# Performance work log

Hardware: AMD Instinct MI355X
Metric: run time of the kernel (lower is better)

## Reference

```python
import jax, jax.numpy as jnp
import numpy as np

N, K, D, H, F = 4, 2048, 512, 8, 2048
Dh = D // H  # per-head dim_q = dim_v = dim_out = 64
EPS = 1e-10


def _uinit(k, shape, fan_sum):
    c = (6.0 / fan_sum) ** 0.5
    return jax.random.uniform(k, shape, jnp.float32, -c, c)


def setup_inputs() -> dict:
    key = jax.random.key(0)
    ks = jax.random.split(key, 8)
    x = jax.random.normal(ks[0], (N, K, D), jnp.float32)
    # per-head projection weights, stacked over heads: (H, D, Dh)
    Wq = _uinit(ks[1], (H, D, Dh), D + Dh)
    Wk = _uinit(ks[2], (H, D, Dh), D + Dh)
    Wv = _uinit(ks[3], (H, D, Dh), D + Dh)
    bq = jnp.zeros((H, Dh), jnp.float32)
    bk = jnp.zeros((H, Dh), jnp.float32)
    bv = jnp.zeros((H, Dh), jnp.float32)
    Wo = _uinit(ks[4], (H * Dh, D), H * Dh + D)
    bo = jnp.zeros((D,), jnp.float32)
    W1 = _uinit(ks[5], (D, F), D + F)
    b1 = jnp.zeros((F,), jnp.float32)
    W2 = _uinit(ks[6], (F, D), F + D)
    b2 = jnp.zeros((D,), jnp.float32)
    g1 = jnp.ones((D,), jnp.float32)
    be1 = jnp.zeros((D,), jnp.float32)
    g2 = jnp.ones((D,), jnp.float32)
    be2 = jnp.zeros((D,), jnp.float32)
    # causal mask: True = masked position (masked_fill semantics)
    mask = jnp.broadcast_to(jnp.triu(jnp.ones((K, K), bool), 1), (N, K, K))
    return dict(x=x, Wq=Wq, bq=bq, Wk=Wk, bk=bk, Wv=Wv, bv=bv, Wo=Wo, bo=bo,
                W1=W1, b1=b1, W2=W2, b2=b2, g1=g1, be1=be1, g2=g2, be2=be2,
                mask=mask)


def _layer_norm(x, g, b):
    m = x.mean(-1, keepdims=True)
    v = ((x - m) ** 2).mean(-1, keepdims=True)
    return g * (x - m) / jnp.sqrt(v + EPS) + b


def _block(x, Wq, bq, Wk, bk, Wv, bv, Wo, bo, W1, b1, W2, b2, g1, be1, g2, be2, mask):
    # per-head projections: (N, H, K, Dh)
    q = jnp.einsum('nkd,hde->nhke', x, Wq) + bq[None, :, None, :]
    k = jnp.einsum('nkd,hde->nhke', x, Wk) + bk[None, :, None, :]
    v = jnp.einsum('nkd,hde->nhke', x, Wv) + bv[None, :, None, :]
    # full score matrix (N, H, K, K) -- faithful to bmm-softmax-bmm
    s = jnp.einsum('nhqe,nhke->nhqk', q, k) / (Dh ** 0.5)
    s = jnp.where(mask[:, None], -1e9, s)
    w = jax.nn.softmax(s, axis=-1)
    att = jnp.einsum('nhqk,nhke->nhqe', w, v)
    att = att.transpose(0, 2, 1, 3).reshape(N, K, H * Dh)  # concat heads
    att = att @ Wo + bo
    h1 = _layer_norm(x + att, g1, be1)
    ff = jax.nn.relu(h1 @ W1 + b1) @ W2 + b2
    return _layer_norm(h1 + ff, g2, be2)


def reference(x, Wq, bq, Wk, bk, Wv, bv, Wo, bo, W1, b1, W2, b2, g1, be1, g2, be2, mask):
    return _block(x, Wq, bq, Wk, bk, Wv, bv, Wo, bo, W1, b1, W2, b2, g1, be1, g2, be2, mask)
```

## Files before the change

### kernel.cpp

```cpp
#include <hip/hip_runtime.h>
#include <cstdint>

typedef unsigned short u16;
typedef __bf16 bf16x8 __attribute__((ext_vector_type(8)));
typedef float f32x4 __attribute__((ext_vector_type(4)));
struct __align__(8) U2 { unsigned x, y; };

#define NEG_INF (-__builtin_inff())

__device__ __forceinline__ u16 f2bf(float f) {
  unsigned u = __builtin_bit_cast(unsigned, f);
  u += 0x7FFFu + ((u >> 16) & 1u);
  return (u16)(u >> 16);
}
__device__ __forceinline__ float bf2f(u16 b) {
  unsigned u = (unsigned)b << 16;
  return __builtin_bit_cast(float, u);
}
__device__ __forceinline__ u16 bfbits(__bf16 x) { return __builtin_bit_cast(u16, x); }
__device__ __forceinline__ unsigned pk2(float a, float b) {
  u16 lo = bfbits((__bf16)a), hi = bfbits((__bf16)b);
  return (unsigned)lo | ((unsigned)hi << 16);
}

__device__ __forceinline__ void async16(u16* dst, const u16* src) {
  __builtin_amdgcn_global_load_lds(
      (__attribute__((address_space(1))) void*)(u16*)src,
      (__attribute__((address_space(3))) void*)dst, 16, 0, 0);
}

__global__ __launch_bounds__(256) void k_prep(const float* __restrict__ Wo,
                                              const float* __restrict__ W1,
                                              const float* __restrict__ W2,
                                              const float* __restrict__ Wq,
                                              const float* __restrict__ Wk,
                                              const float* __restrict__ Wv,
                                              const float* __restrict__ bq,
                                              const float* __restrict__ bk,
                                              const float* __restrict__ bv,
                                              const float* __restrict__ x,
                                              u16* __restrict__ WoT,
                                              u16* __restrict__ W1T,
                                              u16* __restrict__ W2T,
                                              u16* __restrict__ WqkvT,
                                              float* __restrict__ bqkv,
                                              u16* __restrict__ xb) {
  const int b = blockIdx.x, tid = threadIdx.x;
  if (b >= 1542) {
    int i = (b - 1542) * 256 + tid;
    const float4* in = (const float4*)x;
    float4 a = in[2 * i], c = in[2 * i + 1];
    uint4 r;
    r.x = (unsigned)f2bf(a.x) | ((unsigned)f2bf(a.y) << 16);
    r.y = (unsigned)f2bf(a.z) | ((unsigned)f2bf(a.w) << 16);
    r.z = (unsigned)f2bf(c.x) | ((unsigned)f2bf(c.y) << 16);
    r.w = (unsigned)f2bf(c.z) | ((unsigned)f2bf(c.w) << 16);
    ((uint4*)xb)[i] = r;
    return;
  }
  if (b >= 1536) {
    int i = (b - 1536) * 256 + tid;
    int m = i >> 9, r = i & 511;
    const float* B = (m == 0) ? bq : (m == 1) ? bk : bv;
    bqkv[i] = B[r];
    return;
  }
  __shared__ float t[32][65];
  const float* ip;
  u16* op;
  int R, C, r0, c0;
  if (b < 128)      { ip = Wo; op = WoT; R = 512;  C = 512;  c0 = (b & 7) * 64;          r0 = (b >> 3) * 32; }
  else if (b < 640) { int i = b - 128; ip = W1; op = W1T; R = 512;  C = 2048; c0 = (i & 31) * 64; r0 = (i >> 5) * 32; }
  else if (b < 1152){ int i = b - 640; ip = W2; op = W2T; R = 2048; C = 512;  c0 = (i & 7) * 64;  r0 = (i >> 3) * 32; }
  else {
    int i = b - 1152;
    int z = i >> 4;
    const float* W = (z < 8) ? Wq : (z < 16) ? Wk : Wv;
    ip = W + (size_t)(z & 7) * 32768;
    op = WqkvT + (size_t)z * 32768;
    R = 512; C = 64; c0 = 0; r0 = (i & 15) * 32;
  }
  int tx = tid & 63, ty = tid >> 6;
#pragma unroll
  for (int i = 0; i < 32; i += 4)
    t[ty + i][tx] = ip[(size_t)(r0 + ty + i) * C + c0 + tx];
  __syncthreads();
  int cx = tid & 31, cy = tid >> 5;
#pragma unroll
  for (int j = 0; j < 64; j += 8)
    op[(size_t)(c0 + cy + j) * R + r0 + cx] = f2bf(t[cx][cy + j]);
}

template <bool DBUF, int EPI, int BN>
__global__ __launch_bounds__(256) void k_gemm(const u16* __restrict__ A,
                                              const u16* __restrict__ BT,
                                              const float* __restrict__ bias,
                                              u16* __restrict__ Cout,
                                              int M, int N, int Kd) {
  constexpr int HALF = 8192 + BN * 64;
  __shared__ __align__(16) u16 lds[DBUF ? 2 * HALF : HALF];
  constexpr int NFR = BN / 32;
  constexpr int BITER = BN / 32;
  const int tid = threadIdx.x, wid = tid >> 6, lane = tid & 63;
  const int lr = lane & 15, lg = lane >> 4;
  const int wr = wid >> 1, wc = wid & 1;
  const int bid = blockIdx.x;
  const int xcd = bid & 7, local = bid >> 3;
  const int tm = (xcd * 8 + (local & 7)) * 128;
  const int tn = (local >> 3) * BN;

  f32x4 acc[4][NFR] = {};

  const int srow = lane >> 3;
  const int kb = (lane & 7) ^ srow;

  auto STAGE = [&](int buf, int kt) {
    u16* base = lds + buf * HALF;
#pragma unroll
    for (int it = 0; it < 4; ++it) {
      int rid = wid * 4 + it;
      int row = rid * 8 + srow;
      async16(base + rid * 512, A + (size_t)(tm + row) * Kd + kt + kb * 8);
    }
#pragma unroll
    for (int it = 0; it < BITER; ++it) {
      int rid = wid * BITER + it;
      int row = rid * 8 + srow;
      async16(base + 8192 + rid * 512, BT + (size_t)(tn + row) * Kd + kt + kb * 8);
    }
  };

  auto COMPUTE = [&](const char* lp) {
#pragma unroll
    for (int ks = 0; ks < 2; ++ks) {
      const int kbyte = ks * 64 + lg * 16;
      bf16x8 af[4], bfr[NFR];
#pragma unroll
      for (int mi = 0; mi < 4; ++mi) {
        int row = wr * 64 + mi * 16 + lr;
        af[mi] = *(const bf16x8*)(lp + row * 128 + (kbyte ^ ((row & 7) << 4)));
      }
#pragma unroll
      for (int nj = 0; nj < NFR; ++nj) {
        int row = wc * (BN / 2) + nj * 16 + lr;
        bfr[nj] = *(const bf16x8*)(lp + 16384 + row * 128 + (kbyte ^ ((row & 7) << 4)));
      }
#pragma unroll
      for (int mi = 0; mi < 4; ++mi)
#pragma unroll
        for (int nj = 0; nj < NFR; ++nj)
          acc[mi][nj] = __builtin_amdgcn_mfma_f32_16x16x32_bf16(af[mi], bfr[nj], acc[mi][nj], 0, 0, 0);
    }
  };

  const int nkt = Kd >> 6;
  if constexpr (DBUF) {
    STAGE(0, 0);
    for (int ki = 0; ki < nkt; ++ki) {
      __builtin_amdgcn_s_barrier();
      if (ki + 1 < nkt) {
        STAGE((ki + 1) & 1, (ki + 1) << 6);
        if constexpr (BN == 128) asm volatile("s_waitcnt vmcnt(8)" ::: "memory");
        else                     asm volatile("s_waitcnt vmcnt(6)" ::: "memory");
      } else {
        asm volatile("s_waitcnt vmcnt(0)" ::: "memory");
      }
      __builtin_amdgcn_s_barrier();
      __builtin_amdgcn_sched_barrier(0);
      COMPUTE((const char*)(lds + (ki & 1) * HALF));
    }
  } else {
    for (int ki = 0; ki < nkt; ++ki) {
      STAGE(0, ki << 6);
      __syncthreads();
      COMPUTE((const char*)lds);
      __syncthreads();
    }
  }

#pragma unroll
  for (int mi = 0; mi < 4; ++mi)
#pragma unroll
    for (int nj = 0; nj < NFR; ++nj) {
      int col = tn + wc * (BN / 2) + nj * 16 + lr;
      float bv = bias[col];
#pragma unroll
      for (int r = 0; r < 4; ++r) {
        int row = tm + wr * 64 + mi * 16 + lg * 4 + r;
        float v = acc[mi][nj][r] + bv;
        if (EPI == 1) v = v > 0.f ? v : 0.f;
        Cout[(size_t)row * N + col] = f2bf(v);
      }
    }
}

__global__ __launch_bounds__(256) void k_attn(const u16* __restrict__ QKV,
                                              u16* __restrict__ att) {
  __shared__ __align__(16) u16 lds[36864];
  const int lin = blockIdx.x;
  const int L = (lin & 7) * 64 + (lin >> 3);
  const int p = L & 15, nh = L >> 4;
  const int n = nh >> 3, h = nh & 7;
  const int tid = threadIdx.x, wid = tid >> 6, lane = tid & 63;
  const int lr = lane & 15, lg = lane >> 4;
  char* lp = (char*)lds;
  const u16* Qp = QKV + (size_t)(n * 2048) * 1536 + h * 64;
  const u16* Kp = Qp + 512;
  const u16* Vp = Qp + 1024;

  const int vkv = (tid & 31) * 2;
  const int vd0 = (tid >> 5) * 8;
  const int pwb = 65536 + wid * 2048;
  const float C2 = 0.18033688011112042f;
  const float B0 = 14.426950408889634f;

  for (int ph = 0; ph < 2; ++ph) {
    const int qc = (ph == 0) ? p : 31 - p;
    const int ntiles = qc + 1;
    const int qw = qc * 64 + wid * 16;
    const int qa = qw + lr;

    bf16x8 qf[2];
#pragma unroll
    for (int ks = 0; ks < 2; ++ks)
      qf[ks] = *(const bf16x8*)(Qp + (size_t)(qw + lr) * 1536 + ks * 32 + lg * 8);

    f32x4 o[4] = {};
    float lpart = 0.f;

    auto STAGE_K = [&](int t, int b) {
      const int kv0 = t * 64;
#pragma unroll
      for (int it = 0; it < 2; ++it) {
        int c = (wid * 2 + it) * 64 + lane;
        int row = c >> 3, ce = ((c & 7) ^ (row & 7)) * 8;
        async16(&lds[b * 4096 + (wid * 2 + it) * 512],
                Kp + (size_t)(kv0 + row) * 1536 + ce);
      }
    };
    auto VLAND = [&](bf16x8 va, bf16x8 vb, int b) {
#pragma unroll
      for (int jj = 0; jj < 8; ++jj) {
        int d = vd0 + jj;
        unsigned pk = (unsigned)bfbits(va[jj]) | ((unsigned)bfbits(vb[jj]) << 16);
        *(unsigned*)(lp + 32768 + b * 8192 + d * 128 + ((vkv * 2) ^ ((d & 7) << 4))) = pk;
      }
    };
    auto COMPUTE = [&](int t, int b) {
      const int kv0 = t * 64;
      f32x4 s[4] = {};
      __builtin_amdgcn_s_setprio(1);
#pragma unroll
      for (int nj = 0; nj < 4; ++nj) {
        int row = nj * 16 + lr;
#pragma unroll
        for (int ks = 0; ks < 2; ++ks) {
          bf16x8 kf = *(const bf16x8*)(lp + b * 8192 + row * 128 +
                                       ((ks * 64 + lg * 16) ^ ((row & 7) << 4)));
          s[nj] = __builtin_amdgcn_mfma_f32_16x16x32_bf16(kf, qf[ks], s[nj], 0, 0, 0);
        }
      }
      __builtin_amdgcn_s_setprio(0);

      if (t == ntiles - 1) {
#pragma unroll
        for (int nj = 0; nj < 4; ++nj) {
          int kvb = kv0 + nj * 16 + lg * 4;
#pragma unroll
          for (int r = 0; r < 4; ++r)
            if (kvb + r > qa) s[nj][r] = NEG_INF;
        }
      }

      float psum = 0.f;
#pragma unroll
      for (int nj = 0; nj < 4; ++nj)
#pragma unroll
        for (int r = 0; r < 4; ++r) {
          float pv = exp2f(fmaf(s[nj][r], C2, -B0));
          s[nj][r] = pv;
          psum += pv;
        }
      lpart += psum;

#pragma unroll
      for (int nj = 0; nj < 4; ++nj) {
        U2 val;
        val.x = pk2(s[nj][0], s[nj][1]);
        val.y = pk2(s[nj][2], s[nj][3]);
        *(U2*)(lp + pwb + lr * 128 + ((nj * 32 + lg * 8) ^ ((lr & 7) << 4))) = val;
      }

      bf16x8 pa[2];
#pragma unroll
      for (int ks = 0; ks < 2; ++ks)
        pa[ks] = *(const bf16x8*)(lp + pwb + lr * 128 +
                                  ((ks * 64 + lg * 16) ^ ((lr & 7) << 4)));
      __builtin_amdgcn_s_setprio(1);
#pragma unroll
      for (int nd = 0; nd < 4; ++nd) {
        int row = nd * 16 + lr;
#pragma unroll
        for (int ks = 0; ks < 2; ++ks) {
          bf16x8 vf = *(const bf16x8*)(lp + 32768 + b * 8192 + row * 128 +
                                       ((ks * 64 + lg * 16) ^ ((row & 7) << 4)));
          o[nd] = __builtin_amdgcn_mfma_f32_16x16x32_bf16(vf, pa[ks], o[nd], 0, 0, 0);
        }
      }
      __builtin_amdgcn_s_setprio(0);
    };

    STAGE_K(0, 0);
    if (ntiles > 1) STAGE_K(1, 1);
    {
      bf16x8 v0 = *(const bf16x8*)(Vp + (size_t)vkv * 1536 + vd0);
      bf16x8 v1 = *(const bf16x8*)(Vp + (size_t)(vkv + 1) * 1536 + vd0);
      VLAND(v0, v1, 0);
      if (ntiles > 1) {
        bf16x8 v2 = *(const bf16x8*)(Vp + (size_t)(64 + vkv) * 1536 + vd0);
        bf16x8 v3 = *(const bf16x8*)(Vp + (size_t)(64 + vkv + 1) * 1536 + vd0);
        VLAND(v2, v3, 1);
      }
    }
    __syncthreads();

    for (int t = 0; t < ntiles; t += 2) {
      const bool pre0 = (t + 2 < ntiles);
      const bool pre1 = (t + 3 < ntiles);
      bf16x8 va0, vb0, va1, vb1;
      if (pre0) {
        STAGE_K(t + 2, (t + 2) & 3);
        va0 = *(const bf16x8*)(Vp + (size_t)((t + 2) * 64 + vkv) * 1536 + vd0);
        vb0 = *(const bf16x8*)(Vp + (size_t)((t + 2) * 64 + vkv + 1) * 1536 + vd0);
      }
      if (pre1) {
        STAGE_K(t + 3, (t + 3) & 3);
        va1 = *(const bf16x8*)(Vp + (size_t)((t + 3) * 64 + vkv) * 1536 + vd0);
        vb1 = *(const bf16x8*)(Vp + (size_t)((t + 3) * 64 + vkv + 1) * 1536 + vd0);
      }

      COMPUTE(t, t & 3);
      if (t + 1 < ntiles) COMPUTE(t + 1, (t + 1) & 3);

      if (pre0) VLAND(va0, vb0, (t + 2) & 3);
      if (pre1) VLAND(va1, vb1, (t + 3) & 3);
      __syncthreads();
    }

    float lsum = lpart;
    lsum += __shfl_xor(lsum, 16);
    lsum += __shfl_xor(lsum, 32);
    float li = 1.0f / lsum;

    u16* ap = att + (size_t)(n * 2048 + qw + lr) * 512 + h * 64 + lg * 4;
#pragma unroll
    for (int nd = 0; nd < 4; ++nd) {
      U2 val;
      val.x = pk2(o[nd][0] * li, o[nd][1] * li);
      val.y = pk2(o[nd][2] * li, o[nd][3] * li);
      *(U2*)(ap + nd * 16) = val;
    }
  }
}

template <bool XF32>
__global__ __launch_bounds__(256) void k_add_ln(const void* __restrict__ Xp,
                                                const u16* __restrict__ Yb,
                                                const float* __restrict__ gam,
                                                const float* __restrict__ bet,
                                                float* __restrict__ outf,
                                                u16* __restrict__ outb) {
  const int wid = threadIdx.x >> 6, lane = threadIdx.x & 63;
  const size_t row = (size_t)blockIdx.x * 4 + wid;
  float xv[8];
  if constexpr (XF32) {
    const float4* x = (const float4*)((const float*)Xp + row * 512);
    float4 a0 = x[lane], a1 = x[lane + 64];
    xv[0] = a0.x; xv[1] = a0.y; xv[2] = a0.z; xv[3] = a0.w;
    xv[4] = a1.x; xv[5] = a1.y; xv[6] = a1.z; xv[7] = a1.w;
  } else {
    const u16* x = (const u16*)Xp + row * 512;
    U2 x0 = *(const U2*)(x + lane * 4);
    U2 x1 = *(const U2*)(x + 256 + lane * 4);
    xv[0] = bf2f((u16)(x0.x & 0xFFFF)); xv[1] = bf2f((u16)(x0.x >> 16));
    xv[2] = bf2f((u16)(x0.y & 0xFFFF)); xv[3] = bf2f((u16)(x0.y >> 16));
    xv[4] = bf2f((u16)(x1.x & 0xFFFF)); xv[5] = bf2f((u16)(x1.x >> 16));
    xv[6] = bf2f((u16)(x1.y & 0xFFFF)); xv[7] = bf2f((u16)(x1.y >> 16));
  }
  U2 y0 = *(const U2*)(Yb + row * 512 + lane * 4);
  U2 y1 = *(const U2*)(Yb + row * 512 + 256 + lane * 4);
  float v[8];
  v[0] = xv[0] + bf2f((u16)(y0.x & 0xFFFF));
  v[1] = xv[1] + bf2f((u16)(y0.x >> 16));
  v[2] = xv[2] + bf2f((u16)(y0.y & 0xFFFF));
  v[3] = xv[3] + bf2f((u16)(y0.y >> 16));
  v[4] = xv[4] + bf2f((u16)(y1.x & 0xFFFF));
  v[5] = xv[5] + bf2f((u16)(y1.x >> 16));
  v[6] = xv[6] + bf2f((u16)(y1.y & 0xFFFF));
  v[7] = xv[7] + bf2f((u16)(y1.y >> 16));
  float s = 0.f, ss = 0.f;
#pragma unroll
  for (int i = 0; i < 8; ++i) { s += v[i]; ss += v[i] * v[i]; }
#pragma unroll
  for (int m = 1; m < 64; m <<= 1) { s += __shfl_xor(s, m); ss += __shfl_xor(ss, m); }
  float mean = s * (1.f / 512.f);
  float var = ss * (1.f / 512.f) - mean * mean;
  float rstd = rsqrtf(var + 1e-10f);
  float4 g0 = ((const float4*)gam)[lane], g1 = ((const float4*)gam)[lane + 64];
  float4 e0 = ((const float4*)bet)[lane], e1 = ((const float4*)bet)[lane + 64];
  float o[8];
  o[0] = g0.x * (v[0] - mean) * rstd + e0.x;
  o[1] = g0.y * (v[1] - mean) * rstd + e0.y;
  o[2] = g0.z * (v[2] - mean) * rstd + e0.z;
  o[3] = g0.w * (v[3] - mean) * rstd + e0.w;
  o[4] = g1.x * (v[4] - mean) * rstd + e1.x;
  o[5] = g1.y * (v[5] - mean) * rstd + e1.y;
  o[6] = g1.z * (v[6] - mean) * rstd + e1.z;
  o[7] = g1.w * (v[7] - mean) * rstd + e1.w;
  if (outf) {
    float4* of = (float4*)(outf + row * 512);
    float4 w0, w1;
    w0.x = o[0]; w0.y = o[1]; w0.z = o[2]; w0.w = o[3];
    w1.x = o[4]; w1.y = o[5]; w1.z = o[6]; w1.w = o[7];
    of[lane] = w0;
    of[lane + 64] = w1;
  }
  if (outb) {
    u16* ob = outb + row * 512;
    U2 p0, p1;
    p0.x = pk2(o[0], o[1]); p0.y = pk2(o[2], o[3]);
    p1.x = pk2(o[4], o[5]); p1.y = pk2(o[6], o[7]);
    *(U2*)(ob + lane * 4) = p0;
    *(U2*)(ob + 256 + lane * 4) = p1;
  }
}

extern "C" void kernel_launch(void* const* d_in, const int* in_sizes, int n_in,
                              void* d_out, int out_size, void* d_ws, size_t ws_size,
                              hipStream_t stream) {
  const float* x  = (const float*)d_in[0];
  const float* Wq = (const float*)d_in[1];
  const float* bq = (const float*)d_in[2];
  const float* Wk = (const float*)d_in[3];
  const float* bk = (const float*)d_in[4];
  const float* Wv = (const float*)d_in[5];
  const float* bv = (const float*)d_in[6];
  const float* Wo = (const float*)d_in[7];
  const float* bo = (const float*)d_in[8];
  const float* W1 = (const float*)d_in[9];
  const float* b1 = (const float*)d_in[10];
  const float* W2 = (const float*)d_in[11];
  const float* b2 = (const float*)d_in[12];
  const float* g1 = (const float*)d_in[13];
  const float* be1 = (const float*)d_in[14];
  const float* g2 = (const float*)d_in[15];
  const float* be2 = (const float*)d_in[16];

  char* ws = (char*)d_ws;
  u16* xb   = (u16*)(ws + 0);
  u16* attb = (u16*)(ws + 0);
  u16* h1b  = (u16*)(ws + 0);
  u16* WqkvT = (u16*)(ws + (size_t)(8u << 20));
  u16* WoT = WqkvT + 786432;
  u16* W1T = WoT + 262144;
  u16* W2T = W1T + 1048576;
  float* bqkv = (float*)(W2T + 1048576);
  u16* QKV = (u16*)(ws + (size_t)(16u << 20));
  u16* attproj = (u16*)(ws + (size_t)(16u << 20));
  u16* ff1 = (u16*)(ws + (size_t)(16u << 20));
  u16* ffn2 = (u16*)(ws + (size_t)(50u << 20));

  k_prep<<<3590, 256, 0, stream>>>(Wo, W1, W2, Wq, Wk, Wv, bq, bk, bv, x,
                                   WoT, W1T, W2T, WqkvT, bqkv, xb);

  k_gemm<true, 0, 128><<<768, 256, 0, stream>>>(xb, WqkvT, bqkv, QKV, 8192, 1536, 512);
  k_attn<<<512, 256, 0, stream>>>(QKV, attb);
  k_gemm<true, 0, 64><<<512, 256, 0, stream>>>(attb, WoT, bo, attproj, 8192, 512, 512);
  k_add_ln<true><<<2048, 256, 0, stream>>>(x, attproj, g1, be1, nullptr, h1b);
  k_gemm<false, 1, 128><<<1024, 256, 0, stream>>>(h1b, W1T, b1, ff1, 8192, 2048, 512);
  k_gemm<true, 0, 64><<<512, 256, 0, stream>>>(ff1, W2T, b2, ffn2, 8192, 512, 2048);
  k_add_ln<false><<<2048, 256, 0, stream>>>(h1b, ffn2, g2, be2, (float*)d_out, nullptr);
}
```

Measured before the change: 156.4 us.

## Add 512-thread 256x128 GEMM for FFN1 and use bf16 residual in LN1

Adds a new k_gemm8 kernel with 512 threads per block, a 256x128 output tile and XCD-aware tile mapping, and uses it for the FFN1 GEMM with ReLU. The larger tile is meant to raise data reuse per LDS load. The first add+LayerNorm now reads the bf16 copy of x instead of fp32 x, which halves its residual read traffic at some cost in precision. The attention output buffer moves to its own workspace region so it no longer overwrites the bf16 x. The vmcnt wait counts in the double-buffered GEMM are also tightened, which makes each iteration wait on more of its outstanding loads.

```diff
diff --git a/kernel.cpp b/kernel.cpp
--- a/kernel.cpp
+++ b/kernel.cpp
@@ -160,8 +160,8 @@
       __builtin_amdgcn_s_barrier();
       if (ki + 1 < nkt) {
         STAGE((ki + 1) & 1, (ki + 1) << 6);
-        if constexpr (BN == 128) asm volatile("s_waitcnt vmcnt(8)" ::: "memory");
-        else                     asm volatile("s_waitcnt vmcnt(6)" ::: "memory");
+        if constexpr (BN == 128) asm volatile("s_waitcnt vmcnt(6)" ::: "memory");
+        else                     asm volatile("s_waitcnt vmcnt(5)" ::: "memory");
       } else {
         asm volatile("s_waitcnt vmcnt(0)" ::: "memory");
       }
@@ -183,6 +183,93 @@
 #pragma unroll
     for (int nj = 0; nj < NFR; ++nj) {
       int col = tn + wc * (BN / 2) + nj * 16 + lr;
+      float bv = bias[col];
+#pragma unroll
+      for (int r = 0; r < 4; ++r) {
+        int row = tm + wr * 64 + mi * 16 + lg * 4 + r;
+        float v = acc[mi][nj][r] + bv;
+        if (EPI == 1) v = v > 0.f ? v : 0.f;
+        Cout[(size_t)row * N + col] = f2bf(v);
+      }
+    }
+}
+
+template <int EPI>
+__global__ __launch_bounds__(512) void k_gemm8(const u16* __restrict__ A,
+                                               const u16* __restrict__ BT,
+                                               const float* __restrict__ bias,
+                                               u16* __restrict__ Cout,
+                                               int M, int N, int Kd, int mpx) {
+  constexpr int HALF = 24576;
+  __shared__ __align__(16) u16 lds[2 * HALF];
+  const int tid = threadIdx.x, wid = tid >> 6, lane = tid & 63;
+  const int lr = lane & 15, lg = lane >> 4;
+  const int wr = wid >> 1, wc = wid & 1;
+  const int bid = blockIdx.x;
+  const int xcd = bid & 7, local = bid >> 3;
+  const int tm = (xcd * mpx + (local % mpx)) * 256;
+  const int tn = (local / mpx) * 128;
+
+  f32x4 acc[4][4] = {};
+  const int srow = lane >> 3;
+  const int kb = (lane & 7) ^ srow;
+
+  auto STAGE = [&](int buf, int kt) {
+    u16* base = lds + buf * HALF;
+#pragma unroll
+    for (int it = 0; it < 4; ++it) {
+      int rid = wid * 4 + it;
+      int row = rid * 8 + srow;
+      async16(base + rid * 512, A + (size_t)(tm + row) * Kd + kt + kb * 8);
+    }
+#pragma unroll
+    for (int it = 0; it < 2; ++it) {
+      int rid = wid * 2 + it;
+      int row = rid * 8 + srow;
+      async16(base + 16384 + rid * 512, BT + (size_t)(tn + row) * Kd + kt + kb * 8);
+    }
+  };
+
+  const int nkt = Kd >> 6;
+  STAGE(0, 0);
+  for (int ki = 0; ki < nkt; ++ki) {
+    __builtin_amdgcn_s_barrier();
+    if (ki + 1 < nkt) {
+      STAGE((ki + 1) & 1, (ki + 1) << 6);
+      asm volatile("s_waitcnt vmcnt(6)" ::: "memory");
+    } else {
+      asm volatile("s_waitcnt vmcnt(0)" ::: "memory");
+    }
+    __builtin_amdgcn_s_barrier();
+    __builtin_amdgcn_sched_barrier(0);
+    const char* lp = (const char*)(lds + (ki & 1) * HALF);
+#pragma unroll
+    for (int ks = 0; ks < 2; ++ks) {
+      const int kbyte = ks * 64 + lg * 16;
+      bf16x8 af[4], bfr[4];
+#pragma unroll
+      for (int mi = 0; mi < 4; ++mi) {
+        int row = wr * 64 + mi * 16 + lr;
+        af[mi] = *(const bf16x8*)(lp + row * 128 + (kbyte ^ ((row & 7) << 4)));
+      }
+#pragma unroll
+      for (int nj = 0; nj < 4; ++nj) {
+        int row = wc * 64 + nj * 16 + lr;
+        bfr[nj] = *(const bf16x8*)(lp + 32768 + row * 128 + (kbyte ^ ((row & 7) << 4)));
+      }
+#pragma unroll
+      for (int mi = 0; mi < 4; ++mi)
+#pragma unroll
+        for (int nj = 0; nj < 4; ++nj)
+          acc[mi][nj] = __builtin_amdgcn_mfma_f32_16x16x32_bf16(af[mi], bfr[nj], acc[mi][nj], 0, 0, 0);
+    }
+  }
+
+#pragma unroll
+  for (int mi = 0; mi < 4; ++mi)
+#pragma unroll
+    for (int nj = 0; nj < 4; ++nj) {
+      int col = tn + wc * 64 + nj * 16 + lr;
       float bv = bias[col];
 #pragma unroll
       for (int r = 0; r < 4; ++r) {
@@ -457,9 +544,8 @@
   const float* be2 = (const float*)d_in[16];
 
   char* ws = (char*)d_ws;
-  u16* xb   = (u16*)(ws + 0);
-  u16* attb = (u16*)(ws + 0);
-  u16* h1b  = (u16*)(ws + 0);
+  u16* xb  = (u16*)(ws + 0);
+  u16* h1b = (u16*)(ws + 0);
   u16* WqkvT = (u16*)(ws + (size_t)(8u << 20));
   u16* WoT = WqkvT + 786432;
   u16* W1T = WoT + 262144;
@@ -468,6 +554,7 @@
   u16* QKV = (u16*)(ws + (size_t)(16u << 20));
   u16* attproj = (u16*)(ws + (size_t)(16u << 20));
   u16* ff1 = (u16*)(ws + (size_t)(16u << 20));
+  u16* attb = (u16*)(ws + (size_t)(40u << 20));
   u16* ffn2 = (u16*)(ws + (size_t)(50u << 20));
 
   k_prep<<<3590, 256, 0, stream>>>(Wo, W1, W2, Wq, Wk, Wv, bq, bk, bv, x,
@@ -476,8 +563,8 @@
   k_gemm<true, 0, 128><<<768, 256, 0, stream>>>(xb, WqkvT, bqkv, QKV, 8192, 1536, 512);
   k_attn<<<512, 256, 0, stream>>>(QKV, attb);
   k_gemm<true, 0, 64><<<512, 256, 0, stream>>>(attb, WoT, bo, attproj, 8192, 512, 512);
-  k_add_ln<true><<<2048, 256, 0, stream>>>(x, attproj, g1, be1, nullptr, h1b);
-  k_gemm<false, 1, 128><<<1024, 256, 0, stream>>>(h1b, W1T, b1, ff1, 8192, 2048, 512);
+  k_add_ln<false><<<2048, 256, 0, stream>>>(xb, attproj, g1, be1, nullptr, h1b);
+  k_gemm8<1><<<512, 512, 0, stream>>>(h1b, W1T, b1, ff1, 8192, 2048, 512, 4);
   k_gemm<true, 0, 64><<<512, 256, 0, stream>>>(ff1, W2T, b2, ffn2, 8192, 512, 2048);
   k_add_ln<false><<<2048, 256, 0, stream>>>(h1b, ffn2, g2, be2, (float*)d_out, nullptr);
 }
```

After: 157.1 us. About the same (+0.4%).
